# Kernel tuning notes

Hardware: AMD Instinct MI355X
Metric: run time of the kernel (lower is better)

Reference implementation:

```python
import jax, jax.numpy as jnp
import numpy as np

B, P, H, D = 32, 512, 512, 512

def setup_inputs() -> dict:
    key = jax.random.key(0)
    k1, k2, k3, k4 = jax.random.split(key, 4)
    px = jax.random.normal(k1, (B, P, D), dtype=jnp.float32)
    hx = jax.random.normal(k2, (B, H, D), dtype=jnp.float32)
    p_mask = jax.random.randint(k3, (B, P), 0, 2) == 1  # True = padded
    h_mask = jax.random.randint(k4, (B, H), 0, 2) == 1
    return {"px": px, "hx": hx, "p_mask": p_mask, "h_mask": h_mask}

def reference(px, hx, p_mask, h_mask):
    # shared (unscaled) score matrix: [B, P, H]
    e = jnp.einsum('bpd,bhd->bph', px, hx)
    neg_inf = jnp.float32(-jnp.inf)
    h_bias = jnp.where(h_mask, neg_inf, 0.0).astype(e.dtype)  # [B, H]
    p_bias = jnp.where(p_mask, neg_inf, 0.0).astype(e.dtype)  # [B, P]
    # softmax over hypothesis axis -> attend px to hx
    weight_b = jax.nn.softmax(e + h_bias[:, None, :], axis=2)  # [B, P, H]
    px_hat = jnp.einsum('bph,bhd->bpd', weight_b, hx)
    # softmax over premise axis -> attend hx to px
    weight_a = jax.nn.softmax(e + p_bias[:, :, None], axis=1)  # [B, P, H]
    hx_hat = jnp.einsum('bph,bpd->bhd', weight_a, px)
    m_p = jnp.concatenate([px, px_hat, px - px_hat, px * px_hat], axis=-1)
    m_h = jnp.concatenate([hx, hx_hat, hx - hx_hat, hx * hx_hat], axis=-1)
    return (m_p, m_h)
```

## Files before the change

### kernel.cpp

```cpp
#include <hip/hip_runtime.h>
#include <math.h>

#define NB 32
#define NN 512
#define ROWC 2048ull

typedef __attribute__((ext_vector_type(8))) short bf16x8;
typedef __attribute__((ext_vector_type(4))) float f32x4;

__device__ __forceinline__ unsigned int fbits(float f) {
  union { float f; unsigned int u; } v; v.f = f; return v.u;
}
__device__ __forceinline__ float bcast(unsigned int u) {
  union { unsigned int u; float f; } v; v.u = u; return v.f;
}
__device__ __forceinline__ unsigned int bf16_rne(float f) {
  unsigned int b = fbits(f);
  return (b + 0x7FFFu + ((b >> 16) & 1u)) >> 16;
}

__device__ __forceinline__ int frag_byte(int blk, int lane, int khalf) {
  int base = ((((khalf << 3) + blk) << 6) + lane) << 4;
  int swz = (blk ^ (lane >> 4) ^ (khalf << 2)) & 7;
  return base ^ (swz << 4);
}

__device__ __forceinline__ void stage_hilo(const float* __restrict__ src, int row0, int k0,
                                           char* __restrict__ Lh, char* __restrict__ Ll,
                                           int t) {
#pragma unroll
  for (int i = 0; i < 8; ++i) {
    int idx = i * 256 + t;
    int r = idx >> 4, c4 = idx & 15;
    int k = c4 << 2;
    float4 f = *(const float4*)&src[(size_t)(row0 + r) * NN + k0 + k];
    unsigned int b0 = fbits(f.x), b1 = fbits(f.y), b2 = fbits(f.z), b3 = fbits(f.w);
    unsigned int h01 = (b0 >> 16) | (b1 & 0xFFFF0000u);
    unsigned int h23 = (b2 >> 16) | (b3 & 0xFFFF0000u);
    float r0 = f.x - bcast(b0 & 0xFFFF0000u);
    float r1 = f.y - bcast(b1 & 0xFFFF0000u);
    float r2 = f.z - bcast(b2 & 0xFFFF0000u);
    float r3 = f.w - bcast(b3 & 0xFFFF0000u);
    unsigned int l01 = (fbits(r0) >> 16) | (fbits(r1) & 0xFFFF0000u);
    unsigned int l23 = (fbits(r2) >> 16) | (fbits(r3) & 0xFFFF0000u);
    int khalf = k >> 5, k8 = (k >> 3) & 3, j = k & 7;
    int byte = frag_byte(r >> 4, (r & 15) + (k8 << 4), khalf) + (j << 1);
    *(uint2*)(Lh + byte) = make_uint2(h01, h23);
    *(uint2*)(Ll + byte) = make_uint2(l01, l23);
  }
}

__global__ __launch_bounds__(256) void gemm_e_stats(
    const float* __restrict__ px, const float* __restrict__ hx,
    const int* __restrict__ p_mask, const int* __restrict__ h_mask,
    float* __restrict__ e,
    float* __restrict__ rpm, float* __restrict__ rps,
    float* __restrict__ cpm, float* __restrict__ cps) {
  __shared__ char Ah[16384], Al[16384], Bh[16384], Bl[16384];
  __shared__ int pmk[128], hmk[128];
  __shared__ float st_m[2][128], st_s[2][128], sc_m[2][128], sc_s[2][128];
  const int b = blockIdx.z;
  const float* A = px + (size_t)b * NN * NN;
  const float* B = hx + (size_t)b * NN * NN;
  float* C = e + (size_t)b * NN * NN;
  const int row0 = blockIdx.y * 128, col0 = blockIdx.x * 128;
  const int t = threadIdx.x;
  const int l = t & 63, w = t >> 6;
  const int wr = w >> 1, wc = w & 1;
  const int g = l >> 4, li = l & 15;

  if (t < 128) pmk[t] = p_mask[(size_t)b * NN + row0 + t];
  else hmk[t - 128] = h_mask[(size_t)b * NN + col0 + (t - 128)];

  f32x4 acc[4][4];
#pragma unroll
  for (int i = 0; i < 4; ++i)
#pragma unroll
    for (int j = 0; j < 4; ++j)
#pragma unroll
      for (int r = 0; r < 4; ++r) acc[i][j][r] = 0.f;

  for (int k0 = 0; k0 < NN; k0 += 64) {
    stage_hilo(A, row0, k0, Ah, Al, t);
    stage_hilo(B, col0, k0, Bh, Bl, t);
    __syncthreads();
#pragma unroll
    for (int kh = 0; kh < 2; ++kh) {
      bf16x8 ah[4], al[4], bh[4], bl[4];
#pragma unroll
      for (int i = 0; i < 4; ++i) {
        int ab = frag_byte(wr * 4 + i, l, kh);
        ah[i] = *(const bf16x8*)(Ah + ab);
        al[i] = *(const bf16x8*)(Al + ab);
        int bb = frag_byte(wc * 4 + i, l, kh);
        bh[i] = *(const bf16x8*)(Bh + bb);
        bl[i] = *(const bf16x8*)(Bl + bb);
      }
#pragma unroll
      for (int i = 0; i < 4; ++i)
#pragma unroll
        for (int j = 0; j < 4; ++j) {
          acc[i][j] = __builtin_amdgcn_mfma_f32_16x16x32_bf16(ah[i], bh[j], acc[i][j], 0, 0, 0);
          acc[i][j] = __builtin_amdgcn_mfma_f32_16x16x32_bf16(ah[i], bl[j], acc[i][j], 0, 0, 0);
          acc[i][j] = __builtin_amdgcn_mfma_f32_16x16x32_bf16(al[i], bh[j], acc[i][j], 0, 0, 0);
        }
    }
    __syncthreads();
  }

#pragma unroll
  for (int i = 0; i < 4; ++i)
#pragma unroll
    for (int j = 0; j < 4; ++j)
#pragma unroll
      for (int r = 0; r < 4; ++r) {
        int row = row0 + wr * 64 + i * 16 + g * 4 + r;
        int col = col0 + wc * 64 + j * 16 + li;
        C[(size_t)row * NN + col] = acc[i][j][r];
      }

#pragma unroll
  for (int i = 0; i < 4; ++i)
#pragma unroll
    for (int r = 0; r < 4; ++r) {
      float v[4];
      float m = -INFINITY;
#pragma unroll
      for (int j = 0; j < 4; ++j) {
        v[j] = hmk[wc * 64 + j * 16 + li] ? -INFINITY : acc[i][j][r];
        m = fmaxf(m, v[j]);
      }
#pragma unroll
      for (int o = 1; o < 16; o <<= 1) m = fmaxf(m, __shfl_xor(m, o));
      float s = 0.f;
#pragma unroll
      for (int j = 0; j < 4; ++j) s += (v[j] == -INFINITY) ? 0.f : __expf(v[j] - m);
#pragma unroll
      for (int o = 1; o < 16; o <<= 1) s += __shfl_xor(s, o);
      if (li == 0) {
        st_m[wc][wr * 64 + i * 16 + g * 4 + r] = m;
        st_s[wc][wr * 64 + i * 16 + g * 4 + r] = s;
      }
    }

#pragma unroll
  for (int j = 0; j < 4; ++j) {
    float v[16];
    float m = -INFINITY;
#pragma unroll
    for (int i = 0; i < 4; ++i)
#pragma unroll
      for (int r = 0; r < 4; ++r) {
        float x = pmk[wr * 64 + i * 16 + g * 4 + r] ? -INFINITY : acc[i][j][r];
        v[i * 4 + r] = x;
        m = fmaxf(m, x);
      }
    m = fmaxf(m, __shfl_xor(m, 16));
    m = fmaxf(m, __shfl_xor(m, 32));
    float s = 0.f;
#pragma unroll
    for (int q = 0; q < 16; ++q) s += (v[q] == -INFINITY) ? 0.f : __expf(v[q] - m);
    s += __shfl_xor(s, 16);
    s += __shfl_xor(s, 32);
    if (g == 0) {
      sc_m[wr][wc * 64 + j * 16 + li] = m;
      sc_s[wr][wc * 64 + j * 16 + li] = s;
    }
  }
  __syncthreads();

  if (t < 128) {
    float m0 = st_m[0][t], m1 = st_m[1][t];
    float s0 = st_s[0][t], s1 = st_s[1][t];
    float m = fmaxf(m0, m1);
    float s = 0.f;
    if (s0 > 0.f) s += s0 * __expf(m0 - m);
    if (s1 > 0.f) s += s1 * __expf(m1 - m);
    rpm[((size_t)b * 4 + blockIdx.x) * NN + row0 + t] = m;
    rps[((size_t)b * 4 + blockIdx.x) * NN + row0 + t] = s;
  } else {
    int c = t - 128;
    float m0 = sc_m[0][c], m1 = sc_m[1][c];
    float s0 = sc_s[0][c], s1 = sc_s[1][c];
    float m = fmaxf(m0, m1);
    float s = 0.f;
    if (s0 > 0.f) s += s0 * __expf(m0 - m);
    if (s1 > 0.f) s += s1 * __expf(m1 - m);
    cpm[((size_t)b * 4 + blockIdx.y) * NN + col0 + c] = m;
    cps[((size_t)b * 4 + blockIdx.y) * NN + col0 + c] = s;
  }
}

__global__ __launch_bounds__(512) void merge_stats(
    const float* __restrict__ rpm, const float* __restrict__ rps,
    const float* __restrict__ cpm, const float* __restrict__ cps,
    float* __restrict__ rmax, float* __restrict__ rinv,
    float* __restrict__ cmax, float* __restrict__ cinv) {
  const int b = blockIdx.x;
  const int t = threadIdx.x;
  const float* pm = blockIdx.y == 0 ? rpm : cpm;
  const float* ps = blockIdx.y == 0 ? rps : cps;
  float* fm = blockIdx.y == 0 ? rmax : cmax;
  float* fi = blockIdx.y == 0 ? rinv : cinv;
  float mj[4], sj[4];
  float m = -INFINITY;
#pragma unroll
  for (int j = 0; j < 4; ++j) {
    mj[j] = pm[((size_t)b * 4 + j) * NN + t];
    sj[j] = ps[((size_t)b * 4 + j) * NN + t];
    m = fmaxf(m, mj[j]);
  }
  float s = 0.f;
#pragma unroll
  for (int j = 0; j < 4; ++j)
    if (sj[j] > 0.f) s += sj[j] * __expf(mj[j] - m);
  fm[(size_t)b * NN + t] = m;
  fi[(size_t)b * NN + t] = 1.0f / s;
}

__global__ __launch_bounds__(256) void gemm_wp(
    const float* __restrict__ E, const float* __restrict__ hxg,
    const float* __restrict__ pxg, const int* __restrict__ h_mask,
    const float* __restrict__ rmax, const float* __restrict__ rinv,
    float* __restrict__ outg) {
  __shared__ union {
    struct { char A[16384]; char B[16384]; } s;
    float ep[64][132];
  } u;
  const int b = blockIdx.z;
  const float* Eb = E + (size_t)b * NN * NN;
  const float* B = hxg + (size_t)b * NN * NN;
  const float* X = pxg + (size_t)b * NN * NN;
  const int* hm = h_mask + (size_t)b * NN;
  const float* rmx = rmax + (size_t)b * NN;
  const float* rin = rinv + (size_t)b * NN;
  float* out = outg + (size_t)b * NN * ROWC;
  const int row0 = blockIdx.y * 128, col0 = blockIdx.x * 128;
  const int t = threadIdx.x;
  const int l = t & 63, w = t >> 6;
  const int wr = w >> 1, wc = w & 1;

  float rmv[8];
#pragma unroll
  for (int i = 0; i < 8; ++i) rmv[i] = rmx[row0 + ((i * 256 + t) >> 4)];

  f32x4 acc[4][4];
#pragma unroll
  for (int i = 0; i < 4; ++i)
#pragma unroll
    for (int j = 0; j < 4; ++j)
#pragma unroll
      for (int r = 0; r < 4; ++r) acc[i][j][r] = 0.f;

  for (int k0 = 0; k0 < NN; k0 += 64) {
#pragma unroll
    for (int i = 0; i < 8; ++i) {
      int idx = i * 256 + t;
      int r = idx >> 4, c4 = idx & 15, k = c4 << 2;
      float4 f = *(const float4*)&Eb[(size_t)(row0 + r) * NN + k0 + k];
      int4 m4 = *(const int4*)&hm[k0 + k];
      float w0 = m4.x ? 0.f : __expf(f.x - rmv[i]);
      float w1 = m4.y ? 0.f : __expf(f.y - rmv[i]);
      float w2 = m4.z ? 0.f : __expf(f.z - rmv[i]);
      float w3 = m4.w ? 0.f : __expf(f.w - rmv[i]);
      unsigned int p01 = bf16_rne(w0) | (bf16_rne(w1) << 16);
      unsigned int p23 = bf16_rne(w2) | (bf16_rne(w3) << 16);
      int khalf = k >> 5, k8 = (k >> 3) & 3, j = k & 7;
      int byte = frag_byte(r >> 4, (r & 15) + (k8 << 4), khalf) + (j << 1);
      *(uint2*)(u.s.A + byte) = make_uint2(p01, p23);
    }
#pragma unroll
    for (int i = 0; i < 4; ++i) {
      int idx = i * 256 + t;
      int kp = idx >> 5, nq = idx & 31;
      int k = kp << 1, n = nq << 2;
      const float* p0 = &B[(size_t)(k0 + k) * NN + col0 + n];
      float4 f0 = *(const float4*)p0;
      float4 f1 = *(const float4*)(p0 + NN);
      int khalf = k >> 5, k8 = (k >> 3) & 3, j = k & 7;
      float fa0[4] = {f0.x, f0.y, f0.z, f0.w};
      float fa1[4] = {f1.x, f1.y, f1.z, f1.w};
#pragma unroll
      for (int c = 0; c < 4; ++c) {
        unsigned int pk = bf16_rne(fa0[c]) | (bf16_rne(fa1[c]) << 16);
        int nn2 = n + c;
        int byte = frag_byte(nn2 >> 4, (nn2 & 15) + (k8 << 4), khalf) + (j << 1);
        *(unsigned int*)(u.s.B + byte) = pk;
      }
    }
    __syncthreads();
#pragma unroll
    for (int kh = 0; kh < 2; ++kh) {
      bf16x8 av[4], bv[4];
#pragma unroll
      for (int i = 0; i < 4; ++i) {
        av[i] = *(const bf16x8*)(u.s.A + frag_byte(wr * 4 + i, l, kh));
        bv[i] = *(const bf16x8*)(u.s.B + frag_byte(wc * 4 + i, l, kh));
      }
#pragma unroll
      for (int i = 0; i < 4; ++i)
#pragma unroll
        for (int j = 0; j < 4; ++j)
          acc[i][j] = __builtin_amdgcn_mfma_f32_16x16x32_bf16(av[i], bv[j], acc[i][j], 0, 0, 0);
    }
    __syncthreads();
  }

  const int g = l >> 4, li = l & 15;
#pragma unroll
  for (int pass = 0; pass < 2; ++pass) {
    if (wr == pass) {
#pragma unroll
      for (int i = 0; i < 4; ++i)
#pragma unroll
        for (int j = 0; j < 4; ++j)
#pragma unroll
          for (int r = 0; r < 4; ++r)
            u.ep[i * 16 + g * 4 + r][wc * 64 + j * 16 + li] = acc[i][j][r];
    }
    __syncthreads();
#pragma unroll
    for (int i = 0; i < 8; ++i) {
      int idx = i * 256 + t;
      int r = idx >> 5, c4 = idx & 31;
      int grow = row0 + pass * 64 + r;
      float ri = rin[grow];
      float4 ph = *(const float4*)&u.ep[r][c4 * 4];
      ph.x *= ri; ph.y *= ri; ph.z *= ri; ph.w *= ri;
      float4 xv = *(const float4*)&X[(size_t)grow * NN + col0 + c4 * 4];
      size_t base = (size_t)grow * ROWC + col0 + c4 * 4;
      *(float4*)&out[base] = xv;
      *(float4*)&out[base + 512] = ph;
      float4 df = {xv.x - ph.x, xv.y - ph.y, xv.z - ph.z, xv.w - ph.w};
      *(float4*)&out[base + 1024] = df;
      float4 pr = {xv.x * ph.x, xv.y * ph.y, xv.z * ph.z, xv.w * ph.w};
      *(float4*)&out[base + 1536] = pr;
    }
    __syncthreads();
  }
}

__global__ __launch_bounds__(256) void gemm_wh(
    const float* __restrict__ E, const float* __restrict__ pxg,
    const float* __restrict__ hxg, const int* __restrict__ p_mask,
    const float* __restrict__ cmax, const float* __restrict__ cinv,
    float* __restrict__ outg) {
  __shared__ union {
    struct { char A[16384]; char B[16384]; } s;
    float ep[64][132];
  } u;
  const int b = blockIdx.z;
  const float* Eb = E + (size_t)b * NN * NN;
  const float* B = pxg + (size_t)b * NN * NN;
  const float* X = hxg + (size_t)b * NN * NN;
  const int* pmsk = p_mask + (size_t)b * NN;
  const float* cmx = cmax + (size_t)b * NN;
  const float* cin = cinv + (size_t)b * NN;
  float* out = outg + (size_t)b * NN * ROWC;
  const int row0 = blockIdx.y * 128, col0 = blockIdx.x * 128;
  const int t = threadIdx.x;
  const int l = t & 63, w = t >> 6;
  const int wr = w >> 1, wc = w & 1;

  float4 cmv[4];
#pragma unroll
  for (int i = 0; i < 4; ++i) {
    int idx = i * 256 + t;
    int n = (idx & 31) << 2;
    cmv[i] = *(const float4*)&cmx[row0 + n];
  }

  f32x4 acc[4][4];
#pragma unroll
  for (int i = 0; i < 4; ++i)
#pragma unroll
    for (int j = 0; j < 4; ++j)
#pragma unroll
      for (int r = 0; r < 4; ++r) acc[i][j][r] = 0.f;

  for (int k0 = 0; k0 < NN; k0 += 64) {
#pragma unroll
    for (int i = 0; i < 4; ++i) {
      int idx = i * 256 + t;
      int kp = idx >> 5, nq = idx & 31;
      int k = kp << 1, n = nq << 2;
      const float* p0 = &Eb[(size_t)(k0 + k) * NN + row0 + n];
      float4 f0 = *(const float4*)p0;
      float4 f1 = *(const float4*)(p0 + NN);
      int pm0 = pmsk[k0 + k], pm1 = pmsk[k0 + k + 1];
      float fa0[4] = {f0.x, f0.y, f0.z, f0.w};
      float fa1[4] = {f1.x, f1.y, f1.z, f1.w};
      float cma[4] = {cmv[i].x, cmv[i].y, cmv[i].z, cmv[i].w};
      int khalf = k >> 5, k8 = (k >> 3) & 3, j = k & 7;
#pragma unroll
      for (int c = 0; c < 4; ++c) {
        float w0 = pm0 ? 0.f : __expf(fa0[c] - cma[c]);
        float w1 = pm1 ? 0.f : __expf(fa1[c] - cma[c]);
        unsigned int pk = bf16_rne(w0) | (bf16_rne(w1) << 16);
        int nn2 = n + c;
        int byte = frag_byte(nn2 >> 4, (nn2 & 15) + (k8 << 4), khalf) + (j << 1);
        *(unsigned int*)(u.s.A + byte) = pk;
      }
    }
#pragma unroll
    for (int i = 0; i < 4; ++i) {
      int idx = i * 256 + t;
      int kp = idx >> 5, nq = idx & 31;
      int k = kp << 1, n = nq << 2;
      const float* p0 = &B[(size_t)(k0 + k) * NN + col0 + n];
      float4 f0 = *(const float4*)p0;
      float4 f1 = *(const float4*)(p0 + NN);
      int khalf = k >> 5, k8 = (k >> 3) & 3, j = k & 7;
      float fa0[4] = {f0.x, f0.y, f0.z, f0.w};
      float fa1[4] = {f1.x, f1.y, f1.z, f1.w};
#pragma unroll
      for (int c = 0; c < 4; ++c) {
        unsigned int pk = bf16_rne(fa0[c]) | (bf16_rne(fa1[c]) << 16);
        int nn2 = n + c;
        int byte = frag_byte(nn2 >> 4, (nn2 & 15) + (k8 << 4), khalf) + (j << 1);
        *(unsigned int*)(u.s.B + byte) = pk;
      }
    }
    __syncthreads();
#pragma unroll
    for (int kh = 0; kh < 2; ++kh) {
      bf16x8 av[4], bv[4];
#pragma unroll
      for (int i = 0; i < 4; ++i) {
        av[i] = *(const bf16x8*)(u.s.A + frag_byte(wr * 4 + i, l, kh));
        bv[i] = *(const bf16x8*)(u.s.B + frag_byte(wc * 4 + i, l, kh));
      }
#pragma unroll
      for (int i = 0; i < 4; ++i)
#pragma unroll
        for (int j = 0; j < 4; ++j)
          acc[i][j] = __builtin_amdgcn_mfma_f32_16x16x32_bf16(av[i], bv[j], acc[i][j], 0, 0, 0);
    }
    __syncthreads();
  }

  const int g = l >> 4, li = l & 15;
#pragma unroll
  for (int pass = 0; pass < 2; ++pass) {
    if (wr == pass) {
#pragma unroll
      for (int i = 0; i < 4; ++i)
#pragma unroll
        for (int j = 0; j < 4; ++j)
#pragma unroll
          for (int r = 0; r < 4; ++r)
            u.ep[i * 16 + g * 4 + r][wc * 64 + j * 16 + li] = acc[i][j][r];
    }
    __syncthreads();
#pragma unroll
    for (int i = 0; i < 8; ++i) {
      int idx = i * 256 + t;
      int r = idx >> 5, c4 = idx & 31;
      int grow = row0 + pass * 64 + r;
      float ci = cin[grow];
      float4 hh = *(const float4*)&u.ep[r][c4 * 4];
      hh.x *= ci; hh.y *= ci; hh.z *= ci; hh.w *= ci;
      float4 xv = *(const float4*)&X[(size_t)grow * NN + col0 + c4 * 4];
      size_t base = (size_t)grow * ROWC + col0 + c4 * 4;
      *(float4*)&out[base] = xv;
      *(float4*)&out[base + 512] = hh;
      float4 df = {xv.x - hh.x, xv.y - hh.y, xv.z - hh.z, xv.w - hh.w};
      *(float4*)&out[base + 1024] = df;
      float4 pr = {xv.x * hh.x, xv.y * hh.y, xv.z * hh.z, xv.w * hh.w};
      *(float4*)&out[base + 1536] = pr;
    }
    __syncthreads();
  }
}

extern "C" void kernel_launch(void* const* d_in, const int* in_sizes, int n_in,
                              void* d_out, int out_size, void* d_ws, size_t ws_size,
                              hipStream_t stream) {
  const float* px = (const float*)d_in[0];
  const float* hx = (const float*)d_in[1];
  const int* p_mask = (const int*)d_in[2];
  const int* h_mask = (const int*)d_in[3];
  float* out = (float*)d_out;

  float* E = (float*)d_ws;
  float* rpm = E + (size_t)NB * NN * NN;
  float* rps = rpm + (size_t)NB * 4 * NN;
  float* cpm = rps + (size_t)NB * 4 * NN;
  float* cps = cpm + (size_t)NB * 4 * NN;
  float* rmaxv = cps + (size_t)NB * 4 * NN;
  float* rinvv = rmaxv + (size_t)NB * NN;
  float* cmaxv = rinvv + (size_t)NB * NN;
  float* cinvv = cmaxv + (size_t)NB * NN;

  dim3 blk(256);
  dim3 gg(4, 4, NB);
  gemm_e_stats<<<gg, blk, 0, stream>>>(px, hx, p_mask, h_mask, E, rpm, rps, cpm, cps);
  merge_stats<<<dim3(NB, 2), dim3(512), 0, stream>>>(rpm, rps, cpm, cps,
                                                     rmaxv, rinvv, cmaxv, cinvv);
  gemm_wp<<<gg, blk, 0, stream>>>(E, hx, px, h_mask, rmaxv, rinvv, out);
  gemm_wh<<<gg, blk, 0, stream>>>(E, px, hx, p_mask, cmaxv, cinvv,
                                  out + (size_t)NB * NN * ROWC);
}
```

Before: 214.8 us.

## Batch global loads before hi/lo split and stage E tile through LDS for coalesced stores

Result: slower. 228.9 us (+6.6%).

```diff
diff --git a/kernel.cpp b/kernel.cpp
--- a/kernel.cpp
+++ b/kernel.cpp
@@ -23,31 +23,6 @@
   int base = ((((khalf << 3) + blk) << 6) + lane) << 4;
   int swz = (blk ^ (lane >> 4) ^ (khalf << 2)) & 7;
   return base ^ (swz << 4);
-}
-
-__device__ __forceinline__ void stage_hilo(const float* __restrict__ src, int row0, int k0,
-                                           char* __restrict__ Lh, char* __restrict__ Ll,
-                                           int t) {
-#pragma unroll
-  for (int i = 0; i < 8; ++i) {
-    int idx = i * 256 + t;
-    int r = idx >> 4, c4 = idx & 15;
-    int k = c4 << 2;
-    float4 f = *(const float4*)&src[(size_t)(row0 + r) * NN + k0 + k];
-    unsigned int b0 = fbits(f.x), b1 = fbits(f.y), b2 = fbits(f.z), b3 = fbits(f.w);
-    unsigned int h01 = (b0 >> 16) | (b1 & 0xFFFF0000u);
-    unsigned int h23 = (b2 >> 16) | (b3 & 0xFFFF0000u);
-    float r0 = f.x - bcast(b0 & 0xFFFF0000u);
-    float r1 = f.y - bcast(b1 & 0xFFFF0000u);
-    float r2 = f.z - bcast(b2 & 0xFFFF0000u);
-    float r3 = f.w - bcast(b3 & 0xFFFF0000u);
-    unsigned int l01 = (fbits(r0) >> 16) | (fbits(r1) & 0xFFFF0000u);
-    unsigned int l23 = (fbits(r2) >> 16) | (fbits(r3) & 0xFFFF0000u);
-    int khalf = k >> 5, k8 = (k >> 3) & 3, j = k & 7;
-    int byte = frag_byte(r >> 4, (r & 15) + (k8 << 4), khalf) + (j << 1);
-    *(uint2*)(Lh + byte) = make_uint2(h01, h23);
-    *(uint2*)(Ll + byte) = make_uint2(l01, l23);
-  }
 }
 
 __global__ __launch_bounds__(256) void gemm_e_stats(
@@ -56,7 +31,10 @@
     float* __restrict__ e,
     float* __restrict__ rpm, float* __restrict__ rps,
     float* __restrict__ cpm, float* __restrict__ cps) {
-  __shared__ char Ah[16384], Al[16384], Bh[16384], Bl[16384];
+  __shared__ union {
+    struct { char Ah[16384]; char Al[16384]; char Bh[16384]; char Bl[16384]; } s;
+    float ep[64][132];
+  } u;
   __shared__ int pmk[128], hmk[128];
   __shared__ float st_m[2][128], st_s[2][128], sc_m[2][128], sc_s[2][128];
   const int b = blockIdx.z;
@@ -81,8 +59,55 @@
       for (int r = 0; r < 4; ++r) acc[i][j][r] = 0.f;
 
   for (int k0 = 0; k0 < NN; k0 += 64) {
-    stage_hilo(A, row0, k0, Ah, Al, t);
-    stage_hilo(B, col0, k0, Bh, Bl, t);
+    float4 fa[8], fb[8];
+#pragma unroll
+    for (int i = 0; i < 8; ++i) {
+      int idx = i * 256 + t;
+      fa[i] = *(const float4*)&A[(size_t)(row0 + (idx >> 4)) * NN + k0 + ((idx & 15) << 2)];
+    }
+#pragma unroll
+    for (int i = 0; i < 8; ++i) {
+      int idx = i * 256 + t;
+      fb[i] = *(const float4*)&B[(size_t)(col0 + (idx >> 4)) * NN + k0 + ((idx & 15) << 2)];
+    }
+#pragma unroll
+    for (int i = 0; i < 8; ++i) {
+      int idx = i * 256 + t;
+      int r = idx >> 4, k = (idx & 15) << 2;
+      float4 f = fa[i];
+      unsigned int b0 = fbits(f.x), b1 = fbits(f.y), b2 = fbits(f.z), b3 = fbits(f.w);
+      unsigned int h01 = (b0 >> 16) | (b1 & 0xFFFF0000u);
+      unsigned int h23 = (b2 >> 16) | (b3 & 0xFFFF0000u);
+      float r0 = f.x - bcast(b0 & 0xFFFF0000u);
+      float r1 = f.y - bcast(b1 & 0xFFFF0000u);
+      float r2 = f.z - bcast(b2 & 0xFFFF0000u);
+      float r3 = f.w - bcast(b3 & 0xFFFF0000u);
+      unsigned int l01 = (fbits(r0) >> 16) | (fbits(r1) & 0xFFFF0000u);
+      unsigned int l23 = (fbits(r2) >> 16) | (fbits(r3) & 0xFFFF0000u);
+      int khalf = k >> 5, k8 = (k >> 3) & 3, j = k & 7;
+      int byte = frag_byte(r >> 4, (r & 15) + (k8 << 4), khalf) + (j << 1);
+      *(uint2*)&u.s.Ah[byte] = make_uint2(h01, h23);
+      *(uint2*)&u.s.Al[byte] = make_uint2(l01, l23);
+    }
+#pragma unroll
+    for (int i = 0; i < 8; ++i) {
+      int idx = i * 256 + t;
+      int r = idx >> 4, k = (idx & 15) << 2;
+      float4 f = fb[i];
+      unsigned int b0 = fbits(f.x), b1 = fbits(f.y), b2 = fbits(f.z), b3 = fbits(f.w);
+      unsigned int h01 = (b0 >> 16) | (b1 & 0xFFFF0000u);
+      unsigned int h23 = (b2 >> 16) | (b3 & 0xFFFF0000u);
+      float r0 = f.x - bcast(b0 & 0xFFFF0000u);
+      float r1 = f.y - bcast(b1 & 0xFFFF0000u);
+      float r2 = f.z - bcast(b2 & 0xFFFF0000u);
+      float r3 = f.w - bcast(b3 & 0xFFFF0000u);
+      unsigned int l01 = (fbits(r0) >> 16) | (fbits(r1) & 0xFFFF0000u);
+      unsigned int l23 = (fbits(r2) >> 16) | (fbits(r3) & 0xFFFF0000u);
+      int khalf = k >> 5, k8 = (k >> 3) & 3, j = k & 7;
+      int byte = frag_byte(r >> 4, (r & 15) + (k8 << 4), khalf) + (j << 1);
+      *(uint2*)&u.s.Bh[byte] = make_uint2(h01, h23);
+      *(uint2*)&u.s.Bl[byte] = make_uint2(l01, l23);
+    }
     __syncthreads();
 #pragma unroll
     for (int kh = 0; kh < 2; ++kh) {
@@ -90,11 +115,11 @@
 #pragma unroll
       for (int i = 0; i < 4; ++i) {
         int ab = frag_byte(wr * 4 + i, l, kh);
-        ah[i] = *(const bf16x8*)(Ah + ab);
-        al[i] = *(const bf16x8*)(Al + ab);
+        ah[i] = *(const bf16x8*)&u.s.Ah[ab];
+        al[i] = *(const bf16x8*)&u.s.Al[ab];
         int bb = frag_byte(wc * 4 + i, l, kh);
-        bh[i] = *(const bf16x8*)(Bh + bb);
-        bl[i] = *(const bf16x8*)(Bl + bb);
+        bh[i] = *(const bf16x8*)&u.s.Bh[bb];
+        bl[i] = *(const bf16x8*)&u.s.Bl[bb];
       }
 #pragma unroll
       for (int i = 0; i < 4; ++i)
@@ -107,17 +132,6 @@
     }
     __syncthreads();
   }
-
-#pragma unroll
-  for (int i = 0; i < 4; ++i)
-#pragma unroll
-    for (int j = 0; j < 4; ++j)
-#pragma unroll
-      for (int r = 0; r < 4; ++r) {
-        int row = row0 + wr * 64 + i * 16 + g * 4 + r;
-        int col = col0 + wc * 64 + j * 16 + li;
-        C[(size_t)row * NN + col] = acc[i][j][r];
-      }
 
 #pragma unroll
   for (int i = 0; i < 4; ++i)
@@ -188,6 +202,29 @@
     if (s1 > 0.f) s += s1 * __expf(m1 - m);
     cpm[((size_t)b * 4 + blockIdx.y) * NN + col0 + c] = m;
     cps[((size_t)b * 4 + blockIdx.y) * NN + col0 + c] = s;
+  }
+
+#pragma unroll
+  for (int pass = 0; pass < 2; ++pass) {
+    __syncthreads();
+    if (wr == pass) {
+#pragma unroll
+      for (int i = 0; i < 4; ++i)
+#pragma unroll
+        for (int j = 0; j < 4; ++j)
+#pragma unroll
+          for (int r = 0; r < 4; ++r)
+            u.ep[i * 16 + g * 4 + r][wc * 64 + j * 16 + li] = acc[i][j][r];
+    }
+    __syncthreads();
+#pragma unroll
+    for (int i = 0; i < 8; ++i) {
+      int idx = i * 256 + t;
+      int r = idx >> 5, c4 = idx & 31;
+      int grow = row0 + pass * 64 + r;
+      float4 v = *(const float4*)&u.ep[r][c4 * 4];
+      *(float4*)&C[(size_t)grow * NN + col0 + c4 * 4] = v;
+    }
   }
 }
 
@@ -267,7 +304,7 @@
       unsigned int p23 = bf16_rne(w2) | (bf16_rne(w3) << 16);
       int khalf = k >> 5, k8 = (k >> 3) & 3, j = k & 7;
       int byte = frag_byte(r >> 4, (r & 15) + (k8 << 4), khalf) + (j << 1);
-      *(uint2*)(u.s.A + byte) = make_uint2(p01, p23);
+      *(uint2*)&u.s.A[byte] = make_uint2(p01, p23);
     }
 #pragma unroll
     for (int i = 0; i < 4; ++i) {
@@ -285,7 +322,7 @@
         unsigned int pk = bf16_rne(fa0[c]) | (bf16_rne(fa1[c]) << 16);
         int nn2 = n + c;
         int byte = frag_byte(nn2 >> 4, (nn2 & 15) + (k8 << 4), khalf) + (j << 1);
-        *(unsigned int*)(u.s.B + byte) = pk;
+        *(unsigned int*)&u.s.B[byte] = pk;
       }
     }
     __syncthreads();
@@ -294,8 +331,8 @@
       bf16x8 av[4], bv[4];
 #pragma unroll
       for (int i = 0; i < 4; ++i) {
-        av[i] = *(const bf16x8*)(u.s.A + frag_byte(wr * 4 + i, l, kh));
-        bv[i] = *(const bf16x8*)(u.s.B + frag_byte(wc * 4 + i, l, kh));
+        av[i] = *(const bf16x8*)&u.s.A[frag_byte(wr * 4 + i, l, kh)];
+        bv[i] = *(const bf16x8*)&u.s.B[frag_byte(wc * 4 + i, l, kh)];
       }
 #pragma unroll
       for (int i = 0; i < 4; ++i)
@@ -399,7 +436,7 @@
         unsigned int pk = bf16_rne(w0) | (bf16_rne(w1) << 16);
         int nn2 = n + c;
         int byte = frag_byte(nn2 >> 4, (nn2 & 15) + (k8 << 4), khalf) + (j << 1);
-        *(unsigned int*)(u.s.A + byte) = pk;
+        *(unsigned int*)&u.s.A[byte] = pk;
       }
     }
 #pragma unroll
@@ -418,7 +455,7 @@
         unsigned int pk = bf16_rne(fa0[c]) | (bf16_rne(fa1[c]) << 16);
         int nn2 = n + c;
         int byte = frag_byte(nn2 >> 4, (nn2 & 15) + (k8 << 4), khalf) + (j << 1);
-        *(unsigned int*)(u.s.B + byte) = pk;
+        *(unsigned int*)&u.s.B[byte] = pk;
       }
     }
     __syncthreads();
@@ -427,8 +464,8 @@
       bf16x8 av[4], bv[4];
 #pragma unroll
       for (int i = 0; i < 4; ++i) {
-        av[i] = *(const bf16x8*)(u.s.A + frag_byte(wr * 4 + i, l, kh));
-        bv[i] = *(const bf16x8*)(u.s.B + frag_byte(wc * 4 + i, l, kh));
+        av[i] = *(const bf16x8*)&u.s.A[frag_byte(wr * 4 + i, l, kh)];
+        bv[i] = *(const bf16x8*)&u.s.B[frag_byte(wc * 4 + i, l, kh)];
       }
 #pragma unroll
       for (int i = 0; i < 4; ++i)
```
